# Kernel tuning notes

Measured on AMD Instinct MI355X. Metric: run time of the kernel, lower is better.

The kernel has to match this reference:

```python
import jax, jax.numpy as jnp
import numpy as np

LBDA = 0.5  # soft-min temperature, default in OTAM_cum_dist_v2


def setup_inputs() -> dict:
    key = jax.random.key(0)
    # frame-similarity distances [n_queries, n_support, q_len, s_len];
    # in the repo these are 1 - cos_sim, i.e. small non-negative floats
    dists = jnp.abs(jax.random.normal(key, (256, 64, 48, 48), dtype=jnp.float32))
    return {"dists": dists}


def _otam_cum_dist(dists, lbda=LBDA):
    """Faithful vectorized port of OTAM_cum_dist_v2.

    dists: [nq, ns, L, M] -> returns [nq, ns] = cum_dists[:, :, -1, -1]
    The torch code pads the last dim by (1,1) with zeros, then runs a
    soft-DTW-style DP:
      row 0      : running sum along m
      col 0      : stays 0 (never written for l >= 1)
      m == 1     : softmin(prev[0],   prev[1],   cur[0])
      1 < m < -1 : softmin(prev[m-1], cur[m-1])
      m == -1    : softmin(prev[-2],  prev[-1],  cur[-2])
    with softmin(xs) = -lbda * log(sum(exp(-x/lbda))).
    """
    nq, ns, L, M = dists.shape
    B = nq * ns
    d = dists.reshape(B, L, M)
    d = jnp.pad(d, ((0, 0), (0, 0), (1, 1)))  # [B, L, M2], M2 = M + 2
    M2 = M + 2

    # row 0: cum[0, m] = cum[0, m-1] + d[0, m], cum[0, 0] = 0 (d[...,0] is the pad 0)
    row0 = jnp.cumsum(d[:, 0, :], axis=-1)  # [B, M2]

    m_idx = jnp.arange(1, M2)
    # prev[m] participates in the softmin only at the two edge columns
    incl_prev_m = (m_idx == 1) | (m_idx == M2 - 1)  # [M2-1] bool

    def row_step(prev, d_row):
        # prev, d_row: [B, M2]; sequential recurrence along m (cur[m] needs cur[m-1])
        xs = (d_row[:, 1:].T, prev[:, :-1].T, prev[:, 1:].T, incl_prev_m)

        def cell(c_prev, x):
            d_m, p_m1, p_m, inc = x  # [B] each, inc scalar bool
            p_m_eff = jnp.where(inc, p_m, jnp.inf)  # exp(-inf/lbda) = 0 -> excluded
            cand = jnp.stack([p_m1, c_prev, p_m_eff], axis=0)  # [3, B]
            c = d_m - lbda * jax.nn.logsumexp(-cand / lbda, axis=0)
            return c, c

        c0 = jnp.zeros(prev.shape[0], dtype=prev.dtype)  # cur[l, 0] = 0
        _, cur = jax.lax.scan(cell, c0, xs)  # [M2-1, B]
        cur = jnp.concatenate([c0[None, :], cur], axis=0).T  # [B, M2]
        return cur, None

    d_rows = jnp.swapaxes(d, 0, 1)[1:]  # [L-1, B, M2]
    final, _ = jax.lax.scan(row_step, row0, d_rows)  # [B, M2]
    return final[:, -1].reshape(nq, ns)


def reference(dists):
    return _otam_cum_dist(dists, LBDA)
```

## Files before the change

### kernel.cpp

```cpp
#include <hip/hip_runtime.h>


template<int CTRL>
__device__ __forceinline__ float dpp_mov(float src, float old) {
    return __int_as_float(__builtin_amdgcn_update_dpp(
        __float_as_int(old), __float_as_int(src), CTRL, 0xF, 0xF, false));
}

__global__ __launch_bounds__(256, 4) void otam_kernel(const float* __restrict__ dists,
                                                      float* __restrict__ out) {
    const int t = blockIdx.x * 256 + threadIdx.x;
    const int k = t & 15;
    const int prob = t >> 4;

    const float* __restrict__ base =
        dists + (size_t)prob * 2304 + ((k < 12) ? 4 * k : 0);

    float P0, P1, P2, P3;
    float F49 = 0.0f;
    float S = 1.0f;
    int offE = 0;

    auto do_row = [&](float4 q) {
        float a0 = __expf(-2.0f * q.x);
        float a1 = __expf(-2.0f * q.y);
        float a2 = __expf(-2.0f * q.z);
        float a3 = __expf(-2.0f * q.w);

        float Plast = dpp_mov<0x111>(P3, 0.0f);
        float pfirst = (k == 0) ? (S + P0) : Plast;
        float be0 = a0 * pfirst;
        float be1 = a1 * P0;
        float be2 = a2 * P1;
        float be3 = a3 * P2;
        float PoldLast = P3;

        float Ap0 = a0,       Bp0 = be0;
        float Ap1 = a1 * Ap0, Bp1 = fmaf(a1, Bp0, be1);
        float Ap2 = a2 * Ap1, Bp2 = fmaf(a2, Bp1, be2);
        float Ap3 = a3 * Ap2, Bp3 = fmaf(a3, Bp2, be3);

        float A = Ap3, B = Bp3;
        { float Au = dpp_mov<0x111>(A, 1.0f), Bu = dpp_mov<0x111>(B, 0.0f);
          B = fmaf(A, Bu, B); A *= Au; }
        { float Au = dpp_mov<0x112>(A, 1.0f), Bu = dpp_mov<0x112>(B, 0.0f);
          B = fmaf(A, Bu, B); A *= Au; }
        { float Au = dpp_mov<0x114>(A, 1.0f), Bu = dpp_mov<0x114>(B, 0.0f);
          B = fmaf(A, Bu, B); A *= Au; }
        { float Au = dpp_mov<0x118>(A, 1.0f), Bu = dpp_mov<0x118>(B, 0.0f);
          B = fmaf(A, Bu, B); A *= Au; }

        float incl = fmaf(A, S, B);
        float yin = dpp_mov<0x111>(incl, S);

        P0 = fmaf(Ap0, yin, Bp0);
        P1 = fmaf(Ap1, yin, Bp1);
        P2 = fmaf(Ap2, yin, Bp2);
        P3 = fmaf(Ap3, yin, Bp3);

        F49 = P3 + PoldLast + F49;
    };

    auto renorm = [&]() {
        float m = (k < 12) ? fmaxf(fmaxf(P0, P1), fmaxf(P2, P3)) : 0.0f;
        m = fmaxf(m, dpp_mov<0x111>(m, 0.0f));
        m = fmaxf(m, dpp_mov<0x112>(m, 0.0f));
        m = fmaxf(m, dpp_mov<0x114>(m, 0.0f));
        m = fmaxf(m, dpp_mov<0x118>(m, 0.0f));
        float g = __int_as_float(__builtin_amdgcn_ds_swizzle(__float_as_int(m), 0x170));
        unsigned e = (__float_as_uint(g) >> 23) & 0xFFu;
        float sc = __uint_as_float((254u - e) << 23);
        offE += (int)e - 127;
        P0 *= sc; P1 *= sc; P2 *= sc; P3 *= sc; F49 *= sc; S *= sc;
    };

    float4 A0, A1, A2, A3, B0, B1, B2, B3, C0, C1, C2, C3;

#define LOADBUF(X, blk) do {                                   \
        const float* _p = base + (blk) * 192;                  \
        X##0 = *(const float4*)(_p);                           \
        X##1 = *(const float4*)(_p + 48);                      \
        X##2 = *(const float4*)(_p + 96);                      \
        X##3 = *(const float4*)(_p + 144);                     \
    } while (0)

    LOADBUF(A, 0);
    LOADBUF(B, 1);
    LOADBUF(C, 2);

    {
        float a0 = __expf(-2.0f * A0.x);
        float a1 = __expf(-2.0f * A0.y);
        float a2 = __expf(-2.0f * A0.z);
        float a3 = __expf(-2.0f * A0.w);
        float Ap0 = a0, Ap1 = Ap0 * a1, Ap2 = Ap1 * a2, Ap3 = Ap2 * a3;
        float A = Ap3;
        A *= dpp_mov<0x111>(A, 1.0f);
        A *= dpp_mov<0x112>(A, 1.0f);
        A *= dpp_mov<0x114>(A, 1.0f);
        A *= dpp_mov<0x118>(A, 1.0f);
        float yin = dpp_mov<0x111>(A, 1.0f);
        P0 = Ap0 * yin; P1 = Ap1 * yin; P2 = Ap2 * yin; P3 = Ap3 * yin;
        F49 = P3;
    }
    do_row(A1); do_row(A2); do_row(A3);
    renorm();
    LOADBUF(A, 3);

#pragma unroll
    for (int r = 0; r < 4; ++r) {
        const int b = 3 * r;
        if (b + 1 < 12) {
            do_row(B0); do_row(B1); do_row(B2); do_row(B3);
            renorm();
            if (b + 4 < 12) LOADBUF(B, b + 4);
        }
        if (b + 2 < 12) {
            do_row(C0); do_row(C1); do_row(C2); do_row(C3);
            renorm();
            if (b + 5 < 12) LOADBUF(C, b + 5);
        }
        if (b + 3 < 12) {
            do_row(A0); do_row(A1); do_row(A2); do_row(A3);
            if (b + 3 < 11) renorm();
            if (b + 6 < 12) LOADBUF(A, b + 6);
        }
    }
#undef LOADBUF

    if (k == 11) {
        out[prob] = -0.5f * (logf(F49) + (float)offE * 0.6931471805599453f);
    }
}

extern "C" void kernel_launch(void* const* d_in, const int* in_sizes, int n_in,
                              void* d_out, int out_size, void* d_ws, size_t ws_size,
                              hipStream_t stream) {
    const float* dists = (const float*)d_in[0];
    float* out = (float*)d_out;
    otam_kernel<<<dim3(1024), dim3(256), 0, stream>>>(dists, out);
}
```

Baseline: 210.9 us.

## Spread 48 columns over all 16 lanes with 3 columns each

Re-partitions each 48-column DP row across all 16 lanes (3 columns per lane) instead of 12 active lanes with 4 columns, which removes idle lanes and shortens the per-lane serial chain. The float4 loads become scalar loads, since 3*k offsets are not 16-byte aligned. Renormalisation now runs every other block, using butterfly DPP max reductions in place of the row-shift plus ds_swizzle broadcast, and the exponential uses a raw exp2 builtin with the folded constant. The scalar loads may cost more memory instructions, and less frequent renormalisation raises the risk of float range overflow.

```diff
diff --git a/kernel.cpp b/kernel.cpp
--- a/kernel.cpp
+++ b/kernel.cpp
@@ -7,40 +7,45 @@
         __float_as_int(old), __float_as_int(src), CTRL, 0xF, 0xF, false));
 }
 
+__device__ __forceinline__ float fast_exp2(float x) {
+#if __has_builtin(__builtin_amdgcn_exp2f)
+    return __builtin_amdgcn_exp2f(x);
+#else
+    return exp2f(x);
+#endif
+}
+
+#define KEXP (-2.88539008177792681472f)
+
 __global__ __launch_bounds__(256, 4) void otam_kernel(const float* __restrict__ dists,
                                                       float* __restrict__ out) {
     const int t = blockIdx.x * 256 + threadIdx.x;
     const int k = t & 15;
     const int prob = t >> 4;
 
-    const float* __restrict__ base =
-        dists + (size_t)prob * 2304 + ((k < 12) ? 4 * k : 0);
+    const float* __restrict__ base = dists + (size_t)prob * 2304 + 3 * k;
 
-    float P0, P1, P2, P3;
+    float P0, P1, P2;
     float F49 = 0.0f;
     float S = 1.0f;
     int offE = 0;
 
-    auto do_row = [&](float4 q) {
-        float a0 = __expf(-2.0f * q.x);
-        float a1 = __expf(-2.0f * q.y);
-        float a2 = __expf(-2.0f * q.z);
-        float a3 = __expf(-2.0f * q.w);
+    auto do_row = [&](float qx, float qy, float qz) {
+        float a0 = fast_exp2(KEXP * qx);
+        float a1 = fast_exp2(KEXP * qy);
+        float a2 = fast_exp2(KEXP * qz);
 
-        float Plast = dpp_mov<0x111>(P3, 0.0f);
-        float pfirst = (k == 0) ? (S + P0) : Plast;
-        float be0 = a0 * pfirst;
+        float Plast = dpp_mov<0x111>(P2, S + P0);
+        float be0 = a0 * Plast;
         float be1 = a1 * P0;
         float be2 = a2 * P1;
-        float be3 = a3 * P2;
-        float PoldLast = P3;
+        float PoldLast = P2;
 
         float Ap0 = a0,       Bp0 = be0;
         float Ap1 = a1 * Ap0, Bp1 = fmaf(a1, Bp0, be1);
         float Ap2 = a2 * Ap1, Bp2 = fmaf(a2, Bp1, be2);
-        float Ap3 = a3 * Ap2, Bp3 = fmaf(a3, Bp2, be3);
 
-        float A = Ap3, B = Bp3;
+        float A = Ap2, B = Bp2;
         { float Au = dpp_mov<0x111>(A, 1.0f), Bu = dpp_mov<0x111>(B, 0.0f);
           B = fmaf(A, Bu, B); A *= Au; }
         { float Au = dpp_mov<0x112>(A, 1.0f), Bu = dpp_mov<0x112>(B, 0.0f);
@@ -56,32 +61,39 @@
         P0 = fmaf(Ap0, yin, Bp0);
         P1 = fmaf(Ap1, yin, Bp1);
         P2 = fmaf(Ap2, yin, Bp2);
-        P3 = fmaf(Ap3, yin, Bp3);
 
-        F49 = P3 + PoldLast + F49;
+        F49 = P2 + PoldLast + F49;
     };
 
     auto renorm = [&]() {
-        float m = (k < 12) ? fmaxf(fmaxf(P0, P1), fmaxf(P2, P3)) : 0.0f;
-        m = fmaxf(m, dpp_mov<0x111>(m, 0.0f));
-        m = fmaxf(m, dpp_mov<0x112>(m, 0.0f));
-        m = fmaxf(m, dpp_mov<0x114>(m, 0.0f));
-        m = fmaxf(m, dpp_mov<0x118>(m, 0.0f));
-        float g = __int_as_float(__builtin_amdgcn_ds_swizzle(__float_as_int(m), 0x170));
-        unsigned e = (__float_as_uint(g) >> 23) & 0xFFu;
+        float m = fmaxf(fmaxf(P0, P1), P2);
+        m = fmaxf(m, dpp_mov<0xB1>(m, m));
+        m = fmaxf(m, dpp_mov<0x4E>(m, m));
+        m = fmaxf(m, dpp_mov<0x141>(m, m));
+        m = fmaxf(m, dpp_mov<0x140>(m, m));
+        unsigned e = (__float_as_uint(m) >> 23) & 0xFFu;
         float sc = __uint_as_float((254u - e) << 23);
         offE += (int)e - 127;
-        P0 *= sc; P1 *= sc; P2 *= sc; P3 *= sc; F49 *= sc; S *= sc;
+        P0 *= sc; P1 *= sc; P2 *= sc; F49 *= sc; S *= sc;
     };
 
-    float4 A0, A1, A2, A3, B0, B1, B2, B3, C0, C1, C2, C3;
+    float A00, A01, A02, A10, A11, A12, A20, A21, A22, A30, A31, A32;
+    float B00, B01, B02, B10, B11, B12, B20, B21, B22, B30, B31, B32;
+    float C00, C01, C02, C10, C11, C12, C20, C21, C22, C30, C31, C32;
 
 #define LOADBUF(X, blk) do {                                   \
         const float* _p = base + (blk) * 192;                  \
-        X##0 = *(const float4*)(_p);                           \
-        X##1 = *(const float4*)(_p + 48);                      \
-        X##2 = *(const float4*)(_p + 96);                      \
-        X##3 = *(const float4*)(_p + 144);                     \
+        X##00 = _p[0];   X##01 = _p[1];   X##02 = _p[2];       \
+        X##10 = _p[48];  X##11 = _p[49];  X##12 = _p[50];      \
+        X##20 = _p[96];  X##21 = _p[97];  X##22 = _p[98];      \
+        X##30 = _p[144]; X##31 = _p[145]; X##32 = _p[146];     \
+    } while (0)
+
+#define DOBLK(X) do {                                          \
+        do_row(X##00, X##01, X##02);                           \
+        do_row(X##10, X##11, X##12);                           \
+        do_row(X##20, X##21, X##22);                           \
+        do_row(X##30, X##31, X##32);                           \
     } while (0)
 
     LOADBUF(A, 0);
@@ -89,46 +101,45 @@
     LOADBUF(C, 2);
 
     {
-        float a0 = __expf(-2.0f * A0.x);
-        float a1 = __expf(-2.0f * A0.y);
-        float a2 = __expf(-2.0f * A0.z);
-        float a3 = __expf(-2.0f * A0.w);
-        float Ap0 = a0, Ap1 = Ap0 * a1, Ap2 = Ap1 * a2, Ap3 = Ap2 * a3;
-        float A = Ap3;
-        A *= dpp_mov<0x111>(A, 1.0f);
-        A *= dpp_mov<0x112>(A, 1.0f);
-        A *= dpp_mov<0x114>(A, 1.0f);
-        A *= dpp_mov<0x118>(A, 1.0f);
-        float yin = dpp_mov<0x111>(A, 1.0f);
-        P0 = Ap0 * yin; P1 = Ap1 * yin; P2 = Ap2 * yin; P3 = Ap3 * yin;
-        F49 = P3;
+        float a0 = fast_exp2(KEXP * A00);
+        float a1 = fast_exp2(KEXP * A01);
+        float a2 = fast_exp2(KEXP * A02);
+        float Ap0 = a0, Ap1 = Ap0 * a1, Ap2 = Ap1 * a2;
+        float Ax = Ap2;
+        Ax *= dpp_mov<0x111>(Ax, 1.0f);
+        Ax *= dpp_mov<0x112>(Ax, 1.0f);
+        Ax *= dpp_mov<0x114>(Ax, 1.0f);
+        Ax *= dpp_mov<0x118>(Ax, 1.0f);
+        float yin = dpp_mov<0x111>(Ax, 1.0f);
+        P0 = Ap0 * yin; P1 = Ap1 * yin; P2 = Ap2 * yin;
+        F49 = P2;
     }
-    do_row(A1); do_row(A2); do_row(A3);
-    renorm();
+    do_row(A10, A11, A12); do_row(A20, A21, A22); do_row(A30, A31, A32);
     LOADBUF(A, 3);
 
 #pragma unroll
     for (int r = 0; r < 4; ++r) {
         const int b = 3 * r;
-        if (b + 1 < 12) {
-            do_row(B0); do_row(B1); do_row(B2); do_row(B3);
-            renorm();
+        {
+            DOBLK(B);
+            if (((b + 1) & 1) && (b + 1) != 11) renorm();
             if (b + 4 < 12) LOADBUF(B, b + 4);
         }
         if (b + 2 < 12) {
-            do_row(C0); do_row(C1); do_row(C2); do_row(C3);
-            renorm();
+            DOBLK(C);
+            if (((b + 2) & 1) && (b + 2) != 11) renorm();
             if (b + 5 < 12) LOADBUF(C, b + 5);
         }
         if (b + 3 < 12) {
-            do_row(A0); do_row(A1); do_row(A2); do_row(A3);
-            if (b + 3 < 11) renorm();
+            DOBLK(A);
+            if (((b + 3) & 1) && (b + 3) != 11) renorm();
             if (b + 6 < 12) LOADBUF(A, b + 6);
         }
     }
 #undef LOADBUF
+#undef DOBLK
 
-    if (k == 11) {
+    if (k == 15) {
         out[prob] = -0.5f * (logf(F49) + (float)offE * 0.6931471805599453f);
     }
 }
```

After: 210.0 us. No clear change (-0.5%).
